# Kernel optimization log

Hardware: AMD Instinct MI355X
Metric: run time of the kernel (lower is better)

The kernel has to match this reference:

```python
import jax, jax.numpy as jnp
import numpy as np

DIM = 768; NH = 8; G = 14; N = G * G + 1; B = 64; PD = DIM // 16; HID = 4 * DIM
SCOPES = (1, 4, 7)


def _build_adj(fs, scope):
    # windowed adjacency on an fs x fs grid, padded with an always-on ACM (class) token
    idx = np.arange(fs)
    ii, jj = np.meshgrid(idx, idx, indexing='ij')
    ri, rj = ii.ravel(), jj.ravel()
    a = ((np.abs(ri[:, None] - ri[None, :]) <= scope) & (np.abs(rj[:, None] - rj[None, :]) <= scope)).astype(np.float32)
    out = np.ones((fs * fs + 1, fs * fs + 1), np.float32)
    out[1:, 1:] = a
    return out


def _prior_adj():
    # loop=0 -> loop1=loop2=0, repeat = NH//4; heads get [adj1,adj1,adj2,adj2,adj3,adj3,ones,ones]
    rep = NH // 4
    mats = [_build_adj(G, s) for s in SCOPES] + [np.ones((N, N), np.float32)]
    return np.stack([m for m in mats for _ in range(rep)], 0)


def _rel_idx():
    coords = np.stack(np.meshgrid(np.arange(G), np.arange(G), indexing='ij')).reshape(2, -1)
    rel = (coords[:, :, None] - coords[:, None, :]).transpose(1, 2, 0).copy()
    rel[..., 0] += G - 1
    rel[..., 1] += G - 1
    rel[..., 0] *= 2 * G - 1
    idx = rel.sum(-1)
    out = np.full((N, N), (2 * G - 1) ** 2 + 1, np.int32)
    out[1:, 1:] = idx
    return out


def _biases():
    r = np.arange(-G, G + 1)  # arange(1-(G+1), G+1)
    g = np.stack(np.meshgrid(r, r, indexing='ij')).reshape(2, -1).T
    return g.astype(np.float32)  # ((2G+1)^2, 2)


def setup_inputs():
    key = jax.random.key(0)
    ks = iter(jax.random.split(key, 32))
    rn = lambda *s: jax.random.normal(next(ks), s, jnp.float32) * 0.02
    return dict(
        x=jax.random.normal(next(ks), (B, N, DIM), jnp.float32),
        norm1_w=jnp.ones(DIM), norm1_b=jnp.zeros(DIM),
        qkv_w=rn(3 * DIM, DIM),
        scale=10.0 * jnp.ones((NH, 1, 1)),
        pp_w=rn(PD, 2), pp_b=jnp.zeros(PD),
        ln1_w=jnp.ones(PD), ln1_b=jnp.zeros(PD), fcp1_w=rn(PD, PD), fcp1_b=jnp.zeros(PD),
        ln2_w=jnp.ones(PD), ln2_b=jnp.zeros(PD), fcp2_w=rn(PD, PD), fcp2_b=jnp.zeros(PD),
        ln3_w=jnp.ones(PD), ln3_b=jnp.zeros(PD), fcp3_w=rn(NH, PD), fcp3_b=jnp.zeros(NH),
        pre_w=rn(NH, NH) + jnp.eye(NH), post_w=rn(NH, NH) + jnp.eye(NH),
        proj_w=rn(DIM, DIM), proj_b=jnp.zeros(DIM),
        norm2_w=jnp.ones(DIM), norm2_b=jnp.zeros(DIM),
        m1_w=rn(HID, DIM), m1_b=jnp.zeros(HID),
        m2_w=rn(DIM, HID), m2_b=jnp.zeros(DIM),
        prior_adj=jnp.asarray(_prior_adj()),
        biases=jnp.asarray(_biases()),
        rel_idx=jnp.asarray(_rel_idx()),
    )


def _ln(x, w, b, eps=1e-5):
    m = x.mean(-1, keepdims=True)
    v = ((x - m) ** 2).mean(-1, keepdims=True)
    return (x - m) / jnp.sqrt(v + eps) * w + b


def _l2n(x, eps=1e-12):
    return x / jnp.maximum(jnp.linalg.norm(x, axis=-1, keepdims=True), eps)


def reference(x, norm1_w, norm1_b, qkv_w, scale, pp_w, pp_b, ln1_w, ln1_b, fcp1_w, fcp1_b, ln2_w, ln2_b, fcp2_w, fcp2_b, ln3_w, ln3_b, fcp3_w, fcp3_b, pre_w, post_w, proj_w, proj_b, norm2_w, norm2_b, m1_w, m1_b, m2_w, m2_b, prior_adj, biases, rel_idx):
    Bq, Nq, C = x.shape
    d = C // NH
    h = _ln(x, norm1_w, norm1_b)
    qkv = (h @ qkv_w.T).reshape(Bq, Nq, 3, NH, d).transpose(2, 0, 3, 1, 4)
    q, k, v = qkv[0], qkv[1], qkv[2]  # each (B, NH, N, d)
    attn = jnp.einsum('bhnd,bhmd->bhnm', _l2n(q), _l2n(k)) * jnp.minimum(scale, 100.0)[None]
    p = biases @ pp_w.T + pp_b
    p = jax.nn.relu(_ln(p, ln1_w, ln1_b)) @ fcp1_w.T + fcp1_b
    p = jax.nn.relu(_ln(p, ln2_w, ln2_b)) @ fcp2_w.T + fcp2_b
    p = jax.nn.relu(_ln(p, ln3_w, ln3_b)) @ fcp3_w.T + fcp3_b  # (841, NH)
    rpb = p[rel_idx]  # (N, N, NH)
    attn = attn + rpb.transpose(2, 0, 1)[None]
    attn = jnp.einsum('oh,bhnm->bonm', pre_w, attn)  # 1x1 conv over heads (pre-softmax)
    attn = jnp.where(prior_adj[None] > 0, attn, -1e9)
    attn = jax.nn.softmax(attn, axis=-1)
    attn = jnp.einsum('oh,bhnm->bonm', post_w, attn)  # 1x1 conv over heads (post-softmax)
    out = jnp.einsum('bhnm,bhmd->bhnd', attn, v).transpose(0, 2, 1, 3).reshape(Bq, Nq, C)
    x = x + (out @ proj_w.T + proj_b)
    h2 = _ln(x, norm2_w, norm2_b)
    h2 = jax.nn.gelu(h2 @ m1_w.T + m1_b, approximate=False) @ m2_w.T + m2_b
    return x + h2
```

## Files before the change

kernel.cpp:

```cpp
#include <hip/hip_runtime.h>
#include <hip/hip_bf16.h>
#include <math.h>

typedef __hip_bfloat16 bf16;
typedef __attribute__((ext_vector_type(8))) short bf16x8;
typedef __attribute__((ext_vector_type(4))) float f32x4;

__device__ __forceinline__ float b2f(bf16 x){ return __bfloat162float(x); }
__device__ __forceinline__ bf16  f2b(float x){ return __float2bfloat16(x); }

__device__ __forceinline__ void gld16(const bf16* g, bf16* l){
    __builtin_amdgcn_global_load_lds(
        (const __attribute__((address_space(1))) unsigned int*)g,
        (__attribute__((address_space(3))) unsigned int*)l, 16, 0, 0);
}

#define NTOK 197
#define NBATCH 64
#define NHEAD 8
#define DHEAD 96
#define DIMC 768
#define NROWS (NBATCH * NTOK)
#define VTS 200
#define SMS 228

#define OFF_P   0ull
#define OFF_W   32768ull
#define SZ_QKVW 3538944ull
#define SZ_PRJW 1179648ull
#define SZ_M1W  4718592ull
#define SZ_M2W  4718592ull
#define OFF_H   (OFF_W + SZ_QKVW + SZ_PRJW + SZ_M1W + SZ_M2W)
#define SZ_H    19365888ull
#define OFF_Q   (OFF_H + SZ_H)
#define OFF_K   (OFF_Q + SZ_H)
#define OFF_V   (OFF_K + SZ_H)

__global__ __launch_bounds__(256) void w_cvt(const float* __restrict__ s, bf16* __restrict__ d, int n4){
    int i = blockIdx.x*256 + threadIdx.x;
    if (i < n4){
        float4 v = ((const float4*)s)[i];
        bf16 t[4] = {f2b(v.x), f2b(v.y), f2b(v.z), f2b(v.w)};
        ((ushort4*)d)[i] = *(ushort4*)t;
    }
}

__global__ __launch_bounds__(64) void pos_mlp(
    const float* __restrict__ biases, const float* __restrict__ pp_w, const float* __restrict__ pp_b,
    const float* __restrict__ ln1w, const float* __restrict__ ln1b,
    const float* __restrict__ f1w,  const float* __restrict__ f1b,
    const float* __restrict__ ln2w, const float* __restrict__ ln2b,
    const float* __restrict__ f2w,  const float* __restrict__ f2b,
    const float* __restrict__ ln3w, const float* __restrict__ ln3b,
    const float* __restrict__ f3w,  const float* __restrict__ f3b,
    float* __restrict__ pout)
{
    const int row = blockIdx.x, j = threadIdx.x;
    __shared__ float va[48], vb[48];
    float b0 = biases[row*2], b1 = biases[row*2+1];
    if (j < 48) va[j] = b0*pp_w[j*2] + b1*pp_w[j*2+1] + pp_b[j];
    __syncthreads();
    {   float s=0.f, s2=0.f;
        for (int i=0;i<48;i++){ float t=va[i]; s+=t; s2+=t*t; }
        float mean=s*(1.f/48.f), var=s2*(1.f/48.f)-mean*mean, inv=rsqrtf(var+1e-5f);
        float r=0.f;
        if (j < 48){
            r = f1b[j];
            for (int i=0;i<48;i++){
                float t = fmaxf((va[i]-mean)*inv*ln1w[i] + ln1b[i], 0.f);
                r += t * f1w[j*48+i];
            }
        }
        __syncthreads();
        if (j < 48) vb[j] = r;
    }
    __syncthreads();
    {   float s=0.f, s2=0.f;
        for (int i=0;i<48;i++){ float t=vb[i]; s+=t; s2+=t*t; }
        float mean=s*(1.f/48.f), var=s2*(1.f/48.f)-mean*mean, inv=rsqrtf(var+1e-5f);
        float r=0.f;
        if (j < 48){
            r = f2b[j];
            for (int i=0;i<48;i++){
                float t = fmaxf((vb[i]-mean)*inv*ln2w[i] + ln2b[i], 0.f);
                r += t * f2w[j*48+i];
            }
        }
        __syncthreads();
        if (j < 48) va[j] = r;
    }
    __syncthreads();
    {   float s=0.f, s2=0.f;
        for (int i=0;i<48;i++){ float t=va[i]; s+=t; s2+=t*t; }
        float mean=s*(1.f/48.f), var=s2*(1.f/48.f)-mean*mean, inv=rsqrtf(var+1e-5f);
        if (j < 8){
            float r = f3b[j];
            for (int i=0;i<48;i++){
                float t = fmaxf((va[i]-mean)*inv*ln3w[i] + ln3b[i], 0.f);
                r += t * f3w[j*48+i];
            }
            pout[row*8+j] = r;
        }
    }
}

__global__ __launch_bounds__(256) void ln768(
    const float* __restrict__ x, const float* __restrict__ w, const float* __restrict__ b,
    bf16* __restrict__ out)
{
    const int row = blockIdx.x, tid = threadIdx.x;
    const int wv = tid >> 6, ln = tid & 63;
    __shared__ float rs[4], rs2[4];
    const float* xr = x + (size_t)row * DIMC;
    float v0 = xr[tid], v1 = xr[tid+256], v2 = xr[tid+512];
    float s = v0+v1+v2, s2 = v0*v0+v1*v1+v2*v2;
    #pragma unroll
    for (int off=32; off; off>>=1){ s += __shfl_xor(s,off,64); s2 += __shfl_xor(s2,off,64); }
    if (ln == 0){ rs[wv]=s; rs2[wv]=s2; }
    __syncthreads();
    s = rs[0]+rs[1]+rs[2]+rs[3]; s2 = rs2[0]+rs2[1]+rs2[2]+rs2[3];
    float mean = s*(1.f/768.f), var = s2*(1.f/768.f) - mean*mean;
    float inv = rsqrtf(var + 1e-5f);
    size_t base = (size_t)row * DIMC;
    out[base+tid]     = f2b((v0-mean)*inv*w[tid]     + b[tid]);
    out[base+tid+256] = f2b((v1-mean)*inv*w[tid+256] + b[tid+256]);
    out[base+tid+512] = f2b((v2-mean)*inv*w[tid+512] + b[tid+512]);
}

__global__ __launch_bounds__(256) void l2norm_qk(bf16* __restrict__ q, bf16* __restrict__ k)
{
    const int wv = threadIdx.x >> 6, ln = threadIdx.x & 63;
    const size_t NR = (size_t)NBATCH*NHEAD*NTOK;
    size_t row = (size_t)blockIdx.x * 4 + wv;
    bf16* ptr = (row < NR) ? (q + row*DHEAD) : (k + (row-NR)*DHEAD);
    float x0 = b2f(ptr[ln]);
    float x1 = (ln < 32) ? b2f(ptr[64+ln]) : 0.f;
    float ss = x0*x0 + x1*x1;
    #pragma unroll
    for (int off=32; off; off>>=1) ss += __shfl_xor(ss,off,64);
    float inv = 1.f / fmaxf(sqrtf(ss), 1e-12f);
    ptr[ln] = f2b(x0*inv);
    if (ln < 32) ptr[64+ln] = f2b(x1*inv);
}

__global__ __launch_bounds__(256) void attn_mfma(
    const bf16* __restrict__ q, const bf16* __restrict__ k, const bf16* __restrict__ vt,
    const float* __restrict__ p, const float* __restrict__ scale,
    const float* __restrict__ pre_w, const float* __restrict__ post_w,
    bf16* __restrict__ ao)
{
    const int id = blockIdx.x;
    const int r8 = id & 7, t8 = id >> 3;
    const int bx = t8 % 25, b = r8 + 8*(t8/25);
    const int n0 = bx*8;
    const int tid = threadIdx.x, wv = tid>>6, ln = tid&63;
    const int fr = ln&15, fq = ln>>4;
    __shared__ float S[NHEAD*8*SMS];
    __shared__ float s_pre[64], s_post[64], s_sc[8];
    bf16* Sb = (bf16*)S;
    if (tid < 64){ s_pre[tid]=pre_w[tid]; s_post[tid]=post_w[tid]; }
    if (tid < 8)  s_sc[tid] = fminf(scale[tid], 100.f);

    #pragma unroll
    for (int hh=0; hh<2; hh++){
        const int h = wv + hh*4;
        int qr = n0 + fr; if (qr > 196) qr = 196;
        const bf16* qrow = q + ((size_t)(b*NHEAD+h)*NTOK + qr)*DHEAD + fq*8;
        bf16x8 a0 = *(const bf16x8*)(qrow);
        bf16x8 a1 = *(const bf16x8*)(qrow+32);
        bf16x8 a2 = *(const bf16x8*)(qrow+64);
        const bf16* kb0 = k + (size_t)(b*NHEAD+h)*NTOK*DHEAD + fq*8;
        int mr0 = fr;
        const bf16* kr = kb0 + (size_t)mr0*DHEAD;
        bf16x8 kv0 = *(const bf16x8*)(kr);
        bf16x8 kv1 = *(const bf16x8*)(kr+32);
        bf16x8 kv2 = *(const bf16x8*)(kr+64);
        for (int mt=0; mt<13; mt++){
            bf16x8 c0=kv0, c1=kv1, c2=kv2;
            if (mt < 12){
                int nr = (mt+1)*16+fr; if (nr>196) nr=196;
                const bf16* kn = kb0 + (size_t)nr*DHEAD;
                kv0 = *(const bf16x8*)(kn);
                kv1 = *(const bf16x8*)(kn+32);
                kv2 = *(const bf16x8*)(kn+64);
            }
            f32x4 acc = {};
            acc = __builtin_amdgcn_mfma_f32_16x16x32_bf16(a0, c0, acc,0,0,0);
            acc = __builtin_amdgcn_mfma_f32_16x16x32_bf16(a1, c1, acc,0,0,0);
            acc = __builtin_amdgcn_mfma_f32_16x16x32_bf16(a2, c2, acc,0,0,0);
            if (fq < 2){
                #pragma unroll
                for (int i=0;i<4;i++)
                    S[(h*8 + fq*4+i)*SMS + mt*16+fr] = acc[i];
            }
        }
    }
    __syncthreads();

    const int sco[8] = {1,1,4,4,7,7,1000,1000};
    for (int c=tid; c<8*224; c+=256){
        int nq = c/224, m = c - nq*224;
        if (m >= 197){
            #pragma unroll
            for (int o=0;o<8;o++) S[(o*8+nq)*SMS+m] = -1e9f;
            continue;
        }
        int n = n0+nq; if (n > 196) n = 196;
        bool always = (n==0) || (m==0);
        int ri=0, ci=0, rj=0, cj=0;
        if (!always){
            ri=(n-1)/14; ci=(n-1)-ri*14;
            rj=(m-1)/14; cj=(m-1)-rj*14;
        }
        int dr = ri-rj; if (dr<0) dr=-dr;
        int dc = ci-cj; if (dc<0) dc=-dc;
        int idx = always ? 730 : (ri-rj+13)*27 + (ci-cj+13);
        const float* pv = p + idx*8;
        float sh[8];
        #pragma unroll
        for (int h=0;h<8;h++) sh[h] = S[(h*8+nq)*SMS+m]*s_sc[h] + pv[h];
        float ov[8];
        #pragma unroll
        for (int o=0;o<8;o++){
            float v=0.f;
            #pragma unroll
            for (int hh2=0;hh2<8;hh2++) v += s_pre[o*8+hh2]*sh[hh2];
            bool on = always || (dr<=sco[o] && dc<=sco[o]);
            ov[o] = on ? v : -1e9f;
        }
        #pragma unroll
        for (int o=0;o<8;o++) S[(o*8+nq)*SMS+m] = ov[o];
    }
    __syncthreads();

    for (int r = wv*16; r < wv*16+16; r++){
        float* row = &S[r*SMS];
        float mx = -3e38f;
        for (int m=ln; m<224; m+=64) mx = fmaxf(mx, row[m]);
        #pragma unroll
        for (int off=32; off; off>>=1) mx = fmaxf(mx, __shfl_xor(mx,off,64));
        float sum = 0.f;
        for (int m=ln; m<224; m+=64){ float e=__expf(row[m]-mx); row[m]=e; sum+=e; }
        #pragma unroll
        for (int off=32; off; off>>=1) sum += __shfl_xor(sum,off,64);
        float inv = 1.f/sum;
        for (int m=ln; m<224; m+=64) row[m] *= inv;
    }
    __syncthreads();

    float ov[7][8];
    #pragma unroll
    for (int kk=0; kk<7; kk++){
        int c = tid + kk*256;
        if (c < 8*197){
            int nq = c/197, m = c - nq*197;
            float ph[8];
            #pragma unroll
            for (int o=0;o<8;o++) ph[o] = S[(o*8+nq)*SMS+m];
            #pragma unroll
            for (int o2=0;o2<8;o2++){
                float v=0.f;
                #pragma unroll
                for (int o=0;o<8;o++) v += s_post[o2*8+o]*ph[o];
                ov[kk][o2]=v;
            }
        }
    }
    __syncthreads();
    #pragma unroll
    for (int kk=0; kk<7; kk++){
        int c = tid + kk*256;
        if (c < 8*197){
            int nq = c/197, m = c - nq*197;
            #pragma unroll
            for (int o=0;o<8;o++) Sb[(o*8+nq)*456 + m] = f2b(ov[kk][o]);
        }
    }
    for (int i=tid; i<64*32; i+=256){
        int r = i>>5, mm = 197 + (i&31);
        if (mm < 224) Sb[r*456+mm] = f2b(0.f);
    }
    __syncthreads();

    const int frA = fr & 7;
    #pragma unroll
    for (int hh=0; hh<2; hh++){
        const int h = wv + hh*4;
        const bf16* vbase = vt + (size_t)(b*NHEAD+h)*DHEAD*VTS;
        for (int dt=0; dt<6; dt++){
            f32x4 acc = {};
            #pragma unroll
            for (int ks=0; ks<7; ks++){
                const bf16* ap = Sb + (h*8+frA)*456 + ks*32 + fq*8;
                const bf16* bp = vbase + (size_t)(dt*16+fr)*VTS + ks*32 + fq*8;
                acc = __builtin_amdgcn_mfma_f32_16x16x32_bf16(*(const bf16x8*)ap, *(const bf16x8*)bp, acc,0,0,0);
            }
            #pragma unroll
            for (int i=0;i<4;i++){
                int nq = fq*4+i, n = n0+nq;
                if (nq < 8 && n < NTOK)
                    ao[((size_t)b*NTOK+n)*DIMC + h*DHEAD + dt*16+fr] = f2b(acc[i]);
            }
        }
    }
}

enum { EPI_QKV=0, EPI_RES=1, EPI_GELU=2, EPI_ACC=3 };

template<int EPI>
__global__ __launch_bounds__(256) void gemm128(
    const bf16* __restrict__ A, int lda, int M,
    const bf16* __restrict__ B, int ldb,
    int K,
    const float* __restrict__ bias,
    const float* __restrict__ resid,
    float* __restrict__ dst_f,
    bf16* __restrict__ dst_b, int lddb,
    bf16* __restrict__ qo, bf16* __restrict__ ko, bf16* __restrict__ vto)
{
    __shared__ bf16 As[128*32];
    __shared__ bf16 Bs[128*32];
    const int tid = threadIdx.x;
    const int wv = tid >> 6, ln = tid & 63;
    const int fr = ln & 15, fq = ln >> 4;
    const int wr = (wv & 1)*64, wc = (wv >> 1)*64;
    const int m0 = blockIdx.y*128, n0 = blockIdx.x*128;
    const int lnrow = ln >> 2, lncol = (ln & 3)*8;
    f32x4 acc[4][4] = {};
    for (int k0=0; k0<K; k0+=32){
        #pragma unroll
        for (int c=0;c<2;c++){
            int rA = m0 + (c*4+wv)*16 + lnrow;
            if (rA >= M) rA = M-1;
            gld16(A + (size_t)rA*lda + k0 + lncol, &As[(c*4+wv)*16*32]);
            int rB = n0 + (c*4+wv)*16 + lnrow;
            gld16(B + (size_t)rB*ldb + k0 + lncol, &Bs[(c*4+wv)*16*32]);
        }
        __syncthreads();
        bf16x8 af[4], bfv[4];
        #pragma unroll
        for (int i=0;i<4;i++){
            af[i]  = *(const bf16x8*)&As[(wr + i*16 + fr)*32 + fq*8];
            bfv[i] = *(const bf16x8*)&Bs[(wc + i*16 + fr)*32 + fq*8];
        }
        #pragma unroll
        for (int mi=0;mi<4;mi++)
            #pragma unroll
            for (int ni=0;ni<4;ni++)
                acc[mi][ni] = __builtin_amdgcn_mfma_f32_16x16x32_bf16(af[mi], bfv[ni], acc[mi][ni],0,0,0);
        __syncthreads();
    }
    #pragma unroll
    for (int mi=0;mi<4;mi++){
        #pragma unroll
        for (int ni=0;ni<4;ni++){
            #pragma unroll
            for (int i=0;i<4;i++){
                int row = m0 + wr + mi*16 + fq*4 + i;
                int col = n0 + wc + ni*16 + fr;
                if (row >= M) continue;
                float val = acc[mi][ni][i];
                if constexpr (EPI == EPI_QKV){
                    int which = col/768, rem = col - which*768;
                    int hh = rem/96, di = rem - hh*96;
                    int bb = row/NTOK, nn = row - bb*NTOK;
                    if (which == 0)      qo[(((size_t)bb*NHEAD+hh)*NTOK+nn)*DHEAD + di] = f2b(val);
                    else if (which == 1) ko[(((size_t)bb*NHEAD+hh)*NTOK+nn)*DHEAD + di] = f2b(val);
                    else                 vto[(((size_t)bb*NHEAD+hh)*DHEAD+di)*VTS + nn] = f2b(val);
                } else if constexpr (EPI == EPI_RES){
                    dst_f[(size_t)row*DIMC + col] = val + bias[col] + resid[(size_t)row*DIMC + col];
                } else if constexpr (EPI == EPI_GELU){
                    float t = val + bias[col];
                    t = 0.5f*t*(1.f + erff(t*0.70710678118654752f));
                    dst_b[(size_t)row*lddb + col] = f2b(t);
                } else {
                    dst_f[(size_t)row*DIMC + col] += val;
                }
            }
        }
    }
}

extern "C" void kernel_launch(void* const* d_in, const int* in_sizes, int n_in,
                              void* d_out, int out_size, void* d_ws, size_t ws_size,
                              hipStream_t stream)
{
    const float* x        = (const float*)d_in[0];
    const float* norm1_w  = (const float*)d_in[1];
    const float* norm1_b  = (const float*)d_in[2];
    const float* qkv_w    = (const float*)d_in[3];
    const float* scale    = (const float*)d_in[4];
    const float* pp_w     = (const float*)d_in[5];
    const float* pp_b     = (const float*)d_in[6];
    const float* ln1_w    = (const float*)d_in[7];
    const float* ln1_b    = (const float*)d_in[8];
    const float* fcp1_w   = (const float*)d_in[9];
    const float* fcp1_b   = (const float*)d_in[10];
    const float* ln2_w    = (const float*)d_in[11];
    const float* ln2_b    = (const float*)d_in[12];
    const float* fcp2_w   = (const float*)d_in[13];
    const float* fcp2_b   = (const float*)d_in[14];
    const float* ln3_w    = (const float*)d_in[15];
    const float* ln3_b    = (const float*)d_in[16];
    const float* fcp3_w   = (const float*)d_in[17];
    const float* fcp3_b   = (const float*)d_in[18];
    const float* pre_w    = (const float*)d_in[19];
    const float* post_w   = (const float*)d_in[20];
    const float* proj_w   = (const float*)d_in[21];
    const float* proj_b   = (const float*)d_in[22];
    const float* nrm2_w   = (const float*)d_in[23];
    const float* nrm2_b   = (const float*)d_in[24];
    const float* m1_w     = (const float*)d_in[25];
    const float* m1_b     = (const float*)d_in[26];
    const float* m2_w     = (const float*)d_in[27];
    const float* m2_b     = (const float*)d_in[28];
    const float* biases   = (const float*)d_in[30];
    float* out = (float*)d_out;

    char* ws = (char*)d_ws;
    float* p      = (float*)(ws + OFF_P);
    bf16*  qkvw_b = (bf16*)(ws + OFF_W);
    bf16*  prjw_b = (bf16*)(ws + OFF_W + SZ_QKVW);
    bf16*  m1w_b  = (bf16*)(ws + OFF_W + SZ_QKVW + SZ_PRJW);
    bf16*  m2w_b  = (bf16*)(ws + OFF_W + SZ_QKVW + SZ_PRJW + SZ_M1W);
    bf16*  h   = (bf16*)(ws + OFF_H);
    bf16*  qb  = (bf16*)(ws + OFF_Q);
    bf16*  kb  = (bf16*)(ws + OFF_K);
    bf16*  vt  = (bf16*)(ws + OFF_V);
    bf16*  ao  = (bf16*)(ws + OFF_H);
    float* x1  = (float*)(ws + OFF_Q);
    bf16*  h2  = (bf16*)(ws + OFF_V);
    bf16*  mid = (bf16*)(ws + OFF_H);

    w_cvt<<<(2304*768/4+255)/256, 256, 0, stream>>>(qkv_w,  qkvw_b, 2304*768/4);
    w_cvt<<<( 768*768/4+255)/256, 256, 0, stream>>>(proj_w, prjw_b,  768*768/4);
    w_cvt<<<(3072*768/4+255)/256, 256, 0, stream>>>(m1_w,   m1w_b,  3072*768/4);
    w_cvt<<<(3072*768/4+255)/256, 256, 0, stream>>>(m2_w,   m2w_b,  3072*768/4);
    pos_mlp<<<841, 64, 0, stream>>>(biases, pp_w, pp_b, ln1_w, ln1_b, fcp1_w, fcp1_b,
                                    ln2_w, ln2_b, fcp2_w, fcp2_b, ln3_w, ln3_b, fcp3_w, fcp3_b, p);
    ln768<<<NROWS, 256, 0, stream>>>(x, norm1_w, norm1_b, h);
    gemm128<EPI_QKV><<<dim3(18, 99), 256, 0, stream>>>(
        h, DIMC, NROWS, qkvw_b, DIMC, DIMC, nullptr, nullptr, nullptr, nullptr, 0, qb, kb, vt);
    l2norm_qk<<<(NBATCH*NHEAD*NTOK*2)/4, 256, 0, stream>>>(qb, kb);
    attn_mfma<<<1600, 256, 0, stream>>>(qb, kb, vt, p, scale, pre_w, post_w, ao);
    gemm128<EPI_RES><<<dim3(6, 99), 256, 0, stream>>>(
        ao, DIMC, NROWS, prjw_b, DIMC, DIMC, proj_b, x, x1, nullptr, 0, nullptr, nullptr, nullptr);
    ln768<<<NROWS, 256, 0, stream>>>(x1, nrm2_w, nrm2_b, h2);
    for (int c=0; c<4; c++){
        gemm128<EPI_GELU><<<dim3(6, 99), 256, 0, stream>>>(
            h2, DIMC, NROWS, m1w_b + (size_t)c*768*DIMC, DIMC, DIMC, m1_b + c*768,
            nullptr, nullptr, mid, 768, nullptr, nullptr, nullptr);
        if (c < 3)
            gemm128<EPI_ACC><<<dim3(6, 99), 256, 0, stream>>>(
                mid, 768, NROWS, m2w_b + c*768, 3072, 768, nullptr, nullptr, x1, nullptr, 0,
                nullptr, nullptr, nullptr);
        else
            gemm128<EPI_RES><<<dim3(6, 99), 256, 0, stream>>>(
                mid, 768, NROWS, m2w_b + c*768, 3072, 768, m2_b, x1, out, nullptr, 0,
                nullptr, nullptr, nullptr);
    }
    (void)in_sizes; (void)n_in; (void)out_size; (void)ws_size;
}
```

Baseline: 927.5 us.

## Restructure MLP into row-half full-K GEMMs, store x1 in bf16, fuse weight casts

The MLP is reorganised from four 768-wide hidden chunks, each accumulating into an fp32 residual, into two row halves. Each half runs the full 3072-wide GELU GEMM and then one full-K output GEMM that adds bias and residual directly. This removes three read-modify-write passes over the fp32 accumulator. The post-attention residual x1 is stored in bf16, which halves its traffic but loses precision in the residual path. The four weight-conversion launches are merged into one, and the V-transpose and score strides are repadded, with a separate kernel zeroing the V padding.

```diff
diff --git a/kernel.cpp b/kernel.cpp
--- a/kernel.cpp
+++ b/kernel.cpp
@@ -21,8 +21,9 @@
 #define DHEAD 96
 #define DIMC 768
 #define NROWS (NBATCH * NTOK)
-#define VTS 200
-#define SMS 228
+#define VTS 224
+#define SMS 208
+#define MHALF 6304
 
 #define OFF_P   0ull
 #define OFF_W   32768ull
@@ -30,18 +31,32 @@
 #define SZ_PRJW 1179648ull
 #define SZ_M1W  4718592ull
 #define SZ_M2W  4718592ull
-#define OFF_H   (OFF_W + SZ_QKVW + SZ_PRJW + SZ_M1W + SZ_M2W)
+#define OFF_H   14188544ull
 #define SZ_H    19365888ull
-#define OFF_Q   (OFF_H + SZ_H)
-#define OFF_K   (OFF_Q + SZ_H)
-#define OFF_V   (OFF_K + SZ_H)
-
-__global__ __launch_bounds__(256) void w_cvt(const float* __restrict__ s, bf16* __restrict__ d, int n4){
+#define OFF_Q   33554432ull
+#define OFF_K   52920320ull
+#define OFF_V   72286208ull
+
+__global__ __launch_bounds__(256) void w_cvt_all(
+    const float* __restrict__ s0, const float* __restrict__ s1,
+    const float* __restrict__ s2, const float* __restrict__ s3, bf16* __restrict__ d)
+{
     int i = blockIdx.x*256 + threadIdx.x;
-    if (i < n4){
-        float4 v = ((const float4*)s)[i];
-        bf16 t[4] = {f2b(v.x), f2b(v.y), f2b(v.z), f2b(v.w)};
-        ((ushort4*)d)[i] = *(ushort4*)t;
+    const float* s; int off;
+    if (i < 442368){ s=s0; off=i; }
+    else if (i < 589824){ s=s1; off=i-442368; }
+    else if (i < 1179648){ s=s2; off=i-589824; }
+    else { s=s3; off=i-1179648; }
+    float4 v = ((const float4*)s)[off];
+    bf16 t[4] = {f2b(v.x), f2b(v.y), f2b(v.z), f2b(v.w)};
+    ((ushort4*)d)[i] = *(ushort4*)t;
+}
+
+__global__ __launch_bounds__(256) void vt_pad(bf16* __restrict__ vt){
+    int i = blockIdx.x*256 + threadIdx.x;
+    if (i < 49152*27){
+        int r = i/27, c = 197 + (i - r*27);
+        vt[(size_t)r*VTS + c] = f2b(0.f);
     }
 }
 
@@ -104,15 +119,19 @@
     }
 }
 
+__device__ __forceinline__ float ldf(const bf16& x){ return __bfloat162float(x); }
+__device__ __forceinline__ float ldf(const float& x){ return x; }
+
+template<typename TIN>
 __global__ __launch_bounds__(256) void ln768(
-    const float* __restrict__ x, const float* __restrict__ w, const float* __restrict__ b,
+    const TIN* __restrict__ x, const float* __restrict__ w, const float* __restrict__ b,
     bf16* __restrict__ out)
 {
     const int row = blockIdx.x, tid = threadIdx.x;
     const int wv = tid >> 6, ln = tid & 63;
     __shared__ float rs[4], rs2[4];
-    const float* xr = x + (size_t)row * DIMC;
-    float v0 = xr[tid], v1 = xr[tid+256], v2 = xr[tid+512];
+    const TIN* xr = x + (size_t)row * DIMC;
+    float v0 = ldf(xr[tid]), v1 = ldf(xr[tid+256]), v2 = ldf(xr[tid+512]);
     float s = v0+v1+v2, s2 = v0*v0+v1*v1+v2*v2;
     #pragma unroll
     for (int off=32; off; off>>=1){ s += __shfl_xor(s,off,64); s2 += __shfl_xor(s2,off,64); }
@@ -170,8 +189,7 @@
         bf16x8 a1 = *(const bf16x8*)(qrow+32);
         bf16x8 a2 = *(const bf16x8*)(qrow+64);
         const bf16* kb0 = k + (size_t)(b*NHEAD+h)*NTOK*DHEAD + fq*8;
-        int mr0 = fr;
-        const bf16* kr = kb0 + (size_t)mr0*DHEAD;
+        const bf16* kr = kb0 + (size_t)fr*DHEAD;
         bf16x8 kv0 = *(const bf16x8*)(kr);
         bf16x8 kv1 = *(const bf16x8*)(kr+32);
         bf16x8 kv2 = *(const bf16x8*)(kr+64);
@@ -198,8 +216,8 @@
     __syncthreads();
 
     const int sco[8] = {1,1,4,4,7,7,1000,1000};
-    for (int c=tid; c<8*224; c+=256){
-        int nq = c/224, m = c - nq*224;
+    for (int c=tid; c<8*SMS; c+=256){
+        int nq = c/SMS, m = c - nq*SMS;
         if (m >= 197){
             #pragma unroll
             for (int o=0;o<8;o++) S[(o*8+nq)*SMS+m] = -1e9f;
@@ -236,15 +254,15 @@
     for (int r = wv*16; r < wv*16+16; r++){
         float* row = &S[r*SMS];
         float mx = -3e38f;
-        for (int m=ln; m<224; m+=64) mx = fmaxf(mx, row[m]);
+        for (int m=ln; m<SMS; m+=64) mx = fmaxf(mx, row[m]);
         #pragma unroll
         for (int off=32; off; off>>=1) mx = fmaxf(mx, __shfl_xor(mx,off,64));
         float sum = 0.f;
-        for (int m=ln; m<224; m+=64){ float e=__expf(row[m]-mx); row[m]=e; sum+=e; }
+        for (int m=ln; m<SMS; m+=64){ float e=__expf(row[m]-mx); row[m]=e; sum+=e; }
         #pragma unroll
         for (int off=32; off; off>>=1) sum += __shfl_xor(sum,off,64);
         float inv = 1.f/sum;
-        for (int m=ln; m<224; m+=64) row[m] *= inv;
+        for (int m=ln; m<SMS; m+=64) row[m] *= inv;
     }
     __syncthreads();
 
@@ -273,12 +291,12 @@
         if (c < 8*197){
             int nq = c/197, m = c - nq*197;
             #pragma unroll
-            for (int o=0;o<8;o++) Sb[(o*8+nq)*456 + m] = f2b(ov[kk][o]);
-        }
-    }
-    for (int i=tid; i<64*32; i+=256){
-        int r = i>>5, mm = 197 + (i&31);
-        if (mm < 224) Sb[r*456+mm] = f2b(0.f);
+            for (int o=0;o<8;o++) Sb[(o*8+nq)*416 + m] = f2b(ov[kk][o]);
+        }
+    }
+    for (int i=tid; i<64*27; i+=256){
+        int r = i/27, mm = 197 + (i - (i/27)*27);
+        Sb[r*416 + mm] = f2b(0.f);
     }
     __syncthreads();
 
@@ -291,7 +309,7 @@
             f32x4 acc = {};
             #pragma unroll
             for (int ks=0; ks<7; ks++){
-                const bf16* ap = Sb + (h*8+frA)*456 + ks*32 + fq*8;
+                const bf16* ap = Sb + (h*8+frA)*416 + ks*32 + fq*8;
                 const bf16* bp = vbase + (size_t)(dt*16+fr)*VTS + ks*32 + fq*8;
                 acc = __builtin_amdgcn_mfma_f32_16x16x32_bf16(*(const bf16x8*)ap, *(const bf16x8*)bp, acc,0,0,0);
             }
@@ -305,7 +323,7 @@
     }
 }
 
-enum { EPI_QKV=0, EPI_RES=1, EPI_GELU=2, EPI_ACC=3 };
+enum { EPI_QKV=0, EPI_X1=1, EPI_GELU=2, EPI_OUT=3 };
 
 template<int EPI>
 __global__ __launch_bounds__(256) void gemm128(
@@ -313,9 +331,11 @@
     const bf16* __restrict__ B, int ldb,
     int K,
     const float* __restrict__ bias,
-    const float* __restrict__ resid,
+    const float* __restrict__ resid_f,
+    const bf16* __restrict__ resid_b,
     float* __restrict__ dst_f,
     bf16* __restrict__ dst_b, int lddb,
+    int row_off,
     bf16* __restrict__ qo, bf16* __restrict__ ko, bf16* __restrict__ vto)
 {
     __shared__ bf16 As[128*32];
@@ -367,14 +387,15 @@
                     if (which == 0)      qo[(((size_t)bb*NHEAD+hh)*NTOK+nn)*DHEAD + di] = f2b(val);
                     else if (which == 1) ko[(((size_t)bb*NHEAD+hh)*NTOK+nn)*DHEAD + di] = f2b(val);
                     else                 vto[(((size_t)bb*NHEAD+hh)*DHEAD+di)*VTS + nn] = f2b(val);
-                } else if constexpr (EPI == EPI_RES){
-                    dst_f[(size_t)row*DIMC + col] = val + bias[col] + resid[(size_t)row*DIMC + col];
+                } else if constexpr (EPI == EPI_X1){
+                    dst_b[(size_t)row*DIMC + col] = f2b(val + bias[col] + resid_f[(size_t)row*DIMC + col]);
                 } else if constexpr (EPI == EPI_GELU){
                     float t = val + bias[col];
                     t = 0.5f*t*(1.f + erff(t*0.70710678118654752f));
                     dst_b[(size_t)row*lddb + col] = f2b(t);
                 } else {
-                    dst_f[(size_t)row*DIMC + col] += val;
+                    size_t g = (size_t)(row + row_off)*DIMC + col;
+                    dst_f[g] = val + bias[col] + b2f(resid_b[g]);
                 }
             }
         }
@@ -428,36 +449,32 @@
     bf16*  kb  = (bf16*)(ws + OFF_K);
     bf16*  vt  = (bf16*)(ws + OFF_V);
     bf16*  ao  = (bf16*)(ws + OFF_H);
-    float* x1  = (float*)(ws + OFF_Q);
-    bf16*  h2  = (bf16*)(ws + OFF_V);
+    bf16*  x1b = (bf16*)(ws + OFF_V);
+    bf16*  h2  = (bf16*)(ws + OFF_K);
     bf16*  mid = (bf16*)(ws + OFF_H);
 
-    w_cvt<<<(2304*768/4+255)/256, 256, 0, stream>>>(qkv_w,  qkvw_b, 2304*768/4);
-    w_cvt<<<( 768*768/4+255)/256, 256, 0, stream>>>(proj_w, prjw_b,  768*768/4);
-    w_cvt<<<(3072*768/4+255)/256, 256, 0, stream>>>(m1_w,   m1w_b,  3072*768/4);
-    w_cvt<<<(3072*768/4+255)/256, 256, 0, stream>>>(m2_w,   m2w_b,  3072*768/4);
+    w_cvt_all<<<6912, 256, 0, stream>>>(qkv_w, proj_w, m1_w, m2_w, qkvw_b);
     pos_mlp<<<841, 64, 0, stream>>>(biases, pp_w, pp_b, ln1_w, ln1_b, fcp1_w, fcp1_b,
                                     ln2_w, ln2_b, fcp2_w, fcp2_b, ln3_w, ln3_b, fcp3_w, fcp3_b, p);
-    ln768<<<NROWS, 256, 0, stream>>>(x, norm1_w, norm1_b, h);
+    ln768<float><<<NROWS, 256, 0, stream>>>(x, norm1_w, norm1_b, h);
     gemm128<EPI_QKV><<<dim3(18, 99), 256, 0, stream>>>(
-        h, DIMC, NROWS, qkvw_b, DIMC, DIMC, nullptr, nullptr, nullptr, nullptr, 0, qb, kb, vt);
+        h, DIMC, NROWS, qkvw_b, DIMC, DIMC, nullptr, nullptr, nullptr, nullptr,
+        nullptr, 0, 0, qb, kb, vt);
+    vt_pad<<<5184, 256, 0, stream>>>(vt);
     l2norm_qk<<<(NBATCH*NHEAD*NTOK*2)/4, 256, 0, stream>>>(qb, kb);
     attn_mfma<<<1600, 256, 0, stream>>>(qb, kb, vt, p, scale, pre_w, post_w, ao);
-    gemm128<EPI_RES><<<dim3(6, 99), 256, 0, stream>>>(
-        ao, DIMC, NROWS, prjw_b, DIMC, DIMC, proj_b, x, x1, nullptr, 0, nullptr, nullptr, nullptr);
-    ln768<<<NROWS, 256, 0, stream>>>(x1, nrm2_w, nrm2_b, h2);
-    for (int c=0; c<4; c++){
-        gemm128<EPI_GELU><<<dim3(6, 99), 256, 0, stream>>>(
-            h2, DIMC, NROWS, m1w_b + (size_t)c*768*DIMC, DIMC, DIMC, m1_b + c*768,
-            nullptr, nullptr, mid, 768, nullptr, nullptr, nullptr);
-        if (c < 3)
-            gemm128<EPI_ACC><<<dim3(6, 99), 256, 0, stream>>>(
-                mid, 768, NROWS, m2w_b + c*768, 3072, 768, nullptr, nullptr, x1, nullptr, 0,
-                nullptr, nullptr, nullptr);
-        else
-            gemm128<EPI_RES><<<dim3(6, 99), 256, 0, stream>>>(
-                mid, 768, NROWS, m2w_b + c*768, 3072, 768, m2_b, x1, out, nullptr, 0,
-                nullptr, nullptr, nullptr);
+    gemm128<EPI_X1><<<dim3(6, 99), 256, 0, stream>>>(
+        ao, DIMC, NROWS, prjw_b, DIMC, DIMC, proj_b, x, nullptr, nullptr,
+        x1b, 0, 0, nullptr, nullptr, nullptr);
+    ln768<bf16><<<NROWS, 256, 0, stream>>>(x1b, nrm2_w, nrm2_b, h2);
+    for (int c=0; c<2; c++){
+        const int r0 = c*MHALF;
+        gemm128<EPI_GELU><<<dim3(24, 50), 256, 0, stream>>>(
+            h2 + (size_t)r0*DIMC, DIMC, MHALF, m1w_b, DIMC, DIMC, m1_b,
+            nullptr, nullptr, nullptr, mid, 3072, 0, nullptr, nullptr, nullptr);
+        gemm128<EPI_OUT><<<dim3(6, 50), 256, 0, stream>>>(
+            mid, 3072, MHALF, m2w_b, 3072, 3072, m2_b,
+            nullptr, x1b, out, nullptr, 0, r0, nullptr, nullptr, nullptr);
     }
     (void)in_sizes; (void)n_in; (void)out_size; (void)ws_size;
 }
```

New measurement: 891.3 us. 1.04x faster.
